# Optimization experiments

Hardware: AMD Instinct MI355X
Metric: run time of the kernel (lower is better)

Reference implementation:

```python
import jax, jax.numpy as jnp
import numpy as np

BATCH, H, W = 1024, 32, 32
NUM_PIXELS = H * W                 # 1024
NUM_WIRES = 11                     # ceil(log2(1024)) + 1
NUM_LAYERS = 8

_CNOT = jnp.array([[1, 0, 0, 0],
                   [0, 1, 0, 0],
                   [0, 0, 0, 1],
                   [0, 0, 1, 0]], dtype=jnp.complex64)


def setup_inputs() -> dict:
    key = jax.random.key(0)
    k1, k2, k3 = jax.random.split(key, 3)
    image = jax.random.uniform(k1, (BATCH, 1, H, W), dtype=jnp.float32)
    label = jax.random.normal(k2, (BATCH,), dtype=jnp.float32)
    weights = jax.random.normal(k3, (NUM_LAYERS, NUM_WIRES, 3), dtype=jnp.float32) * 0.4
    return {"image": image, "label": label, "weights": weights}


def _apply_1q(state, U, w):
    # state: (B,) + (2,)*n ; U: (2,2) shared or (B,2,2) per-batch
    st = jnp.moveaxis(state, w + 1, -1)
    if U.ndim == 3:
        out = jnp.einsum('bij,b...j->b...i', U, st)
    else:
        out = jnp.einsum('ij,...j->...i', U, st)
    return jnp.moveaxis(out, -1, w + 1)


def _apply_cnot(state, c, t):
    last = state.ndim - 1
    st = jnp.moveaxis(state, (c + 1, t + 1), (last - 1, last))
    sh = st.shape
    st = st.reshape(sh[:-2] + (4,)) @ _CNOT.T
    st = st.reshape(sh)
    return jnp.moveaxis(st, (last - 1, last), (c + 1, t + 1))


def _rot(phi, theta, omega):
    # PennyLane Rot = RZ(omega) RY(theta) RZ(phi)
    c = jnp.cos(theta / 2).astype(jnp.complex64)
    s = jnp.sin(theta / 2).astype(jnp.complex64)
    ep = jnp.exp(-0.5j * (phi + omega))
    em = jnp.exp(0.5j * (phi - omega))
    return jnp.array([[ep * c, -em * s],
                      [jnp.conj(em) * s, jnp.conj(ep) * c]])


def _circuit(image, label, weights):
    B = image.shape[0]
    x = image.reshape(B, NUM_PIXELS)
    # AmplitudeEmbedding(normalize=True) on wires 0..NUM_WIRES-2; ancilla wire in |0>
    psi = x / jnp.linalg.norm(x, axis=1, keepdims=True)
    state = jnp.zeros((B, 2 ** NUM_WIRES), jnp.complex64)
    state = state.at[:, ::2].set(psi.astype(jnp.complex64))  # ancilla = least-significant wire
    state = state.reshape((B,) + (2,) * NUM_WIRES)

    # RX(label) on the last wire (per-batch angle)
    c = jnp.cos(label / 2).astype(jnp.complex64)
    s = (-1j * jnp.sin(label / 2)).astype(jnp.complex64)
    rx = jnp.stack([jnp.stack([c, s], -1), jnp.stack([s, c], -1)], -2)  # (B,2,2)
    state = _apply_1q(state, rx, NUM_WIRES - 1)

    # weights remapped as in the module
    wr = jnp.pi * jnp.tanh(weights)

    # StronglyEntanglingLayers: per layer, Rot on every wire then ring of CNOTs with range r
    for l in range(NUM_LAYERS):
        for q in range(NUM_WIRES):
            state = _apply_1q(state, _rot(wr[l, q, 0], wr[l, q, 1], wr[l, q, 2]), q)
        r = (l % (NUM_WIRES - 1)) + 1
        for q in range(NUM_WIRES):
            state = _apply_cnot(state, q, (q + r) % NUM_WIRES)

    probs = jnp.abs(state.reshape(B, -1)) ** 2          # (B, 2048)
    probs = probs[:, ::2]                               # ancilla == 0 outcomes, (B, 1024)
    out = probs * NUM_PIXELS                            # decode: undo 1/num_pixels scale
    return out.reshape(B, 1, H, W)


def reference(image, label, weights):
    return _circuit(image, label, weights)
```

## Files before the change

kernel.cpp:

```cpp
#include <hip/hip_runtime.h>
#include <math.h>

#define NW 11
#define NL 8
#define NPIX 1024
#define TPB 256

typedef float f2 __attribute__((ext_vector_type(2)));
typedef float f4 __attribute__((ext_vector_type(4)));

struct PermTab { int fe[NL][8]; int d[NL][8]; };

__host__ __device__ inline int fmap_h(int m, int r) {
    for (int q = 0; q < NW; ++q) {
        int pc = 10 - q;
        int qq = q + r; if (qq >= NW) qq -= NW;
        int pt = 10 - qq;
        m ^= ((m >> pc) & 1) << pt;
    }
    return m;
}

__host__ __device__ constexpr int SW(int e) {
    return e ^ (((e >> 3) & 7) << 1) ^ (((e >> 6) & 1) << 3);
}

template<int B>
__device__ __forceinline__ void gate8(f2 (&v)[8], const f2* __restrict__ g) {
    f2 c0 = g[0], c1 = g[1], c2 = g[2], c3 = g[3];
    f2 c4 = g[4], c5 = g[5], c6 = g[6], c7 = g[7];
    #pragma unroll
    for (int s = 0; s < 8; ++s) {
        if (s & B) continue;
        f2 v0 = v[s], v1 = v[s | B];
        f2 w0 = v0.yx, w1 = v1.yx;
        f2 o0 = __builtin_elementwise_fma(c3, w1,
                 __builtin_elementwise_fma(c2, v1,
                  __builtin_elementwise_fma(c1, w0, c0 * v0)));
        f2 o1 = __builtin_elementwise_fma(c7, w1,
                 __builtin_elementwise_fma(c6, v1,
                  __builtin_elementwise_fma(c5, w0, c4 * v0)));
        v[s] = o0; v[s | B] = o1;
    }
}

__global__ void gates_kernel(const float* __restrict__ weights, f2* __restrict__ gw) {
    int t = threadIdx.x;
    if (t < NL * NW) {
        const float* w = weights + t * 3;
        const float PI = 3.14159265358979323846f;
        float phi   = PI * tanhf(w[0]);
        float theta = PI * tanhf(w[1]);
        float omega = PI * tanhf(w[2]);
        float ct = cosf(0.5f * theta), st = sinf(0.5f * theta);
        float a  = 0.5f * (phi + omega), bb = 0.5f * (phi - omega);
        float ca = cosf(a), sa = sinf(a), cb = cosf(bb), sb = sinf(bb);
        float u00r =  ca * ct, u00i = -sa * ct;
        float u01r = -cb * st, u01i = -sb * st;
        float u10r =  cb * st, u10i = -sb * st;
        float u11r =  ca * ct, u11i =  sa * ct;
        f2* g = gw + t * 8;
        g[0] = (f2){u00r, u00r}; g[1] = (f2){-u00i, u00i};
        g[2] = (f2){u01r, u01r}; g[3] = (f2){-u01i, u01i};
        g[4] = (f2){u10r, u10r}; g[5] = (f2){-u10i, u10i};
        g[6] = (f2){u11r, u11r}; g[7] = (f2){-u11i, u11i};
    }
}

__global__ __launch_bounds__(TPB) void pqc_kernel(
    const float* __restrict__ image, const float* __restrict__ label,
    const f2* __restrict__ gw, float* __restrict__ out, PermTab pt)
{
    __shared__ __align__(16) f2 sS[2048];
    __shared__ float sRed[4];

    const int b = blockIdx.x, t = threadIdx.x;

    const f4 x = ((const f4*)(image + (size_t)b * NPIX))[t];
    float ss = x.x * x.x + x.y * x.y + x.z * x.z + x.w * x.w;
    #pragma unroll
    for (int off = 32; off >= 1; off >>= 1) ss += __shfl_down(ss, off);
    if ((t & 63) == 0) sRed[t >> 6] = ss;
    __syncthreads();
    const float inv = 1.0f / sqrtf(sRed[0] + sRed[1] + sRed[2] + sRed[3]);

    const float lab = label[b];
    const float cl = cosf(0.5f * lab), sl = sinf(0.5f * lab);

    f2 v[8];
    {
        float ps[4] = {x.x, x.y, x.z, x.w};
        #pragma unroll
        for (int m = 0; m < 4; ++m) {
            float p = ps[m] * inv;
            v[2 * m]     = (f2){cl * p, 0.f};
            v[2 * m + 1] = (f2){0.f, -sl * p};
        }
    }

    const int swb0 = SW(t << 3);
    const int swb1 = SW((t & 7) | ((t >> 3) << 6));
    const int swb2 = SW((t & 63) | ((t >> 6) << 9));
    const int swb3 = SW(t << 1);

    for (int l = 0; l < NL; ++l) {
        const f2* G = gw + (size_t)l * NW * 8;

        if (l) {
            #pragma unroll
            for (int k = 0; k < 4; ++k) {
                f4 w = *(const f4*)&sS[swb0 ^ SW(2 * k)];
                v[2 * k] = w.xy; v[2 * k + 1] = w.zw;
            }
        }
        gate8<1>(v, G + 10 * 8);
        gate8<2>(v, G +  9 * 8);
        gate8<4>(v, G +  8 * 8);
        #pragma unroll
        for (int k = 0; k < 4; ++k) {
            f4 w; w.xy = v[2 * k]; w.zw = v[2 * k + 1];
            *(f4*)&sS[swb0 ^ SW(2 * k)] = w;
        }
        __syncthreads();

        {
            #pragma unroll
            for (int s = 0; s < 8; ++s) v[s] = sS[swb1 ^ SW(s << 3)];
            gate8<1>(v, G + 7 * 8);
            gate8<2>(v, G + 6 * 8);
            gate8<4>(v, G + 5 * 8);
            #pragma unroll
            for (int s = 0; s < 8; ++s) sS[swb1 ^ SW(s << 3)] = v[s];
        }
        __syncthreads();

        {
            #pragma unroll
            for (int s = 0; s < 8; ++s) v[s] = sS[swb2 ^ SW(s << 6)];
            gate8<1>(v, G + 4 * 8);
            gate8<2>(v, G + 3 * 8);
            gate8<4>(v, G + 2 * 8);
            #pragma unroll
            for (int s = 0; s < 8; ++s) sS[swb2 ^ SW(s << 6)] = v[s];
        }
        __syncthreads();

        {
            #pragma unroll
            for (int k = 0; k < 4; ++k) {
                f4 w = *(const f4*)&sS[swb3 ^ ((k & 1) << 9) ^ ((k >> 1) << 10)];
                v[2 * k] = w.xy; v[2 * k + 1] = w.zw;
            }
            gate8<2>(v, G + 1 * 8);
            gate8<4>(v, G + 0 * 8);
            int msw = 0;
            #pragma unroll
            for (int k2 = 0; k2 < 8; ++k2)
                msw ^= ((t >> k2) & 1) ? pt.fe[l][k2] : 0;
            #pragma unroll
            for (int s = 0; s < 8; ++s) sS[msw ^ pt.d[l][s]] = v[s];
        }
        __syncthreads();
    }

    {
        f4 o;
        #pragma unroll
        for (int k = 0; k < 4; ++k) {
            f2 a = sS[swb0 ^ SW(2 * k)];
            ((float*)&o)[k] = (a.x * a.x + a.y * a.y) * (float)NPIX;
        }
        ((f4*)(out + (size_t)b * NPIX))[t] = o;
    }
}

extern "C" void kernel_launch(void* const* d_in, const int* in_sizes, int n_in,
                              void* d_out, int out_size, void* d_ws, size_t ws_size,
                              hipStream_t stream) {
    const float* image   = (const float*)d_in[0];
    const float* label   = (const float*)d_in[1];
    const float* weights = (const float*)d_in[2];
    float* out = (float*)d_out;
    f2* gw = (f2*)d_ws;

    PermTab pt;
    for (int l = 0; l < NL; ++l) {
        int r = l + 1;
        for (int k = 0; k < 8; ++k)
            pt.fe[l][k] = SW(fmap_h(1 << (k + 1), r));
        for (int s = 0; s < 8; ++s) {
            int m = 0;
            if (s & 1) m ^= fmap_h(1,       r);
            if (s & 2) m ^= fmap_h(1 << 9,  r);
            if (s & 4) m ^= fmap_h(1 << 10, r);
            pt.d[l][s] = SW(m);
        }
    }

    int batch = in_sizes[1];
    gates_kernel<<<1, 128, 0, stream>>>(weights, gw);
    pqc_kernel<<<batch, TPB, 0, stream>>>(image, label, gw, out, pt);
}
```

Measured before the change: 45.06 us.

## Make early layer phases wave-local and double-buffer state to cut block barriers

Rearranges which amplitudes each thread owns so that the first three gate phases of a layer only exchange data within a 64-lane wavefront. This lets those phases use s_waitcnt plus a sched_barrier instead of __syncthreads. Shared state is double-buffered so the permuted CNOT write-back targets the other buffer, which removes one more barrier. Each layer drops from four block barriers to two, at the cost of twice the LDS per block and new swizzle patterns that may cause bank conflicts. Correctness relies on the wave-locality of the index mappings and on wave-synchronous execution.

```diff
diff --git a/kernel.cpp b/kernel.cpp
--- a/kernel.cpp
+++ b/kernel.cpp
@@ -22,7 +22,7 @@
 }
 
 __host__ __device__ constexpr int SW(int e) {
-    return e ^ (((e >> 3) & 7) << 1) ^ (((e >> 6) & 1) << 3);
+    return e ^ (((e >> 6) & 7) << 1);
 }
 
 template<int B>
@@ -71,7 +71,7 @@
     const float* __restrict__ image, const float* __restrict__ label,
     const f2* __restrict__ gw, float* __restrict__ out, PermTab pt)
 {
-    __shared__ __align__(16) f2 sS[2048];
+    __shared__ __align__(16) f2 sS[2 * 2048];
     __shared__ float sRed[4];
 
     const int b = blockIdx.x, t = threadIdx.x;
@@ -98,77 +98,79 @@
         }
     }
 
-    const int swb0 = SW(t << 3);
-    const int swb1 = SW((t & 7) | ((t >> 3) << 6));
-    const int swb2 = SW((t & 63) | ((t >> 6) << 9));
-    const int swb3 = SW(t << 1);
-
+    const int swbA = (((t >> 6) << 9) | ((t & 63) << 3)) ^ (((t >> 3) & 7) << 1);
+    const int swbB = ((t & 7) | (((t >> 3) & 7) << 6) | ((t >> 6) << 9))
+                   ^ (((t >> 3) & 7) << 1);
+    const int swbC = (t & 63) | ((t >> 6) << 9);
+    const int swbD = (t << 1) ^ (((t >> 5) & 7) << 1);
+
+    int offS = 0;
     for (int l = 0; l < NL; ++l) {
         const f2* G = gw + (size_t)l * NW * 8;
+        const int offT = offS ^ 2048;
+        const int bA = offS ^ swbA, bB = offS ^ swbB;
+        const int bC = offS ^ swbC, bD = offS ^ swbD;
 
         if (l) {
             #pragma unroll
-            for (int k = 0; k < 4; ++k) {
-                f4 w = *(const f4*)&sS[swb0 ^ SW(2 * k)];
-                v[2 * k] = w.xy; v[2 * k + 1] = w.zw;
+            for (int j = 0; j < 4; ++j) {
+                f4 w = *(const f4*)&sS[bA ^ (2 * j)];
+                v[2 * j] = w.xy; v[2 * j + 1] = w.zw;
             }
         }
         gate8<1>(v, G + 10 * 8);
         gate8<2>(v, G +  9 * 8);
         gate8<4>(v, G +  8 * 8);
         #pragma unroll
-        for (int k = 0; k < 4; ++k) {
-            f4 w; w.xy = v[2 * k]; w.zw = v[2 * k + 1];
-            *(f4*)&sS[swb0 ^ SW(2 * k)] = w;
-        }
+        for (int j = 0; j < 4; ++j) {
+            f4 w; w.xy = v[2 * j]; w.zw = v[2 * j + 1];
+            *(f4*)&sS[bA ^ (2 * j)] = w;
+        }
+        asm volatile("s_waitcnt lgkmcnt(0)" ::: "memory");
+        __builtin_amdgcn_sched_barrier(0);
+
+        #pragma unroll
+        for (int s = 0; s < 8; ++s) v[s] = sS[bB ^ (s << 3)];
+        gate8<1>(v, G + 7 * 8);
+        gate8<2>(v, G + 6 * 8);
+        gate8<4>(v, G + 5 * 8);
+        #pragma unroll
+        for (int s = 0; s < 8; ++s) sS[bB ^ (s << 3)] = v[s];
+        asm volatile("s_waitcnt lgkmcnt(0)" ::: "memory");
+        __builtin_amdgcn_sched_barrier(0);
+
+        #pragma unroll
+        for (int s = 0; s < 8; ++s) v[s] = sS[bC ^ (s << 6) ^ (s << 1)];
+        gate8<1>(v, G + 4 * 8);
+        gate8<2>(v, G + 3 * 8);
+        gate8<4>(v, G + 2 * 8);
+        #pragma unroll
+        for (int s = 0; s < 8; ++s) sS[bC ^ (s << 6) ^ (s << 1)] = v[s];
         __syncthreads();
 
-        {
-            #pragma unroll
-            for (int s = 0; s < 8; ++s) v[s] = sS[swb1 ^ SW(s << 3)];
-            gate8<1>(v, G + 7 * 8);
-            gate8<2>(v, G + 6 * 8);
-            gate8<4>(v, G + 5 * 8);
-            #pragma unroll
-            for (int s = 0; s < 8; ++s) sS[swb1 ^ SW(s << 3)] = v[s];
-        }
+        #pragma unroll
+        for (int j = 0; j < 4; ++j) {
+            f4 w = *(const f4*)&sS[bD ^ ((j & 1) << 9) ^ ((j >> 1) << 10)];
+            v[2 * j] = w.xy; v[2 * j + 1] = w.zw;
+        }
+        gate8<2>(v, G + 1 * 8);
+        gate8<4>(v, G + 0 * 8);
+        int msw = offT;
+        #pragma unroll
+        for (int k2 = 0; k2 < 8; ++k2)
+            msw ^= ((t >> k2) & 1) ? pt.fe[l][k2] : 0;
+        #pragma unroll
+        for (int s = 0; s < 8; ++s) sS[msw ^ pt.d[l][s]] = v[s];
         __syncthreads();
-
-        {
-            #pragma unroll
-            for (int s = 0; s < 8; ++s) v[s] = sS[swb2 ^ SW(s << 6)];
-            gate8<1>(v, G + 4 * 8);
-            gate8<2>(v, G + 3 * 8);
-            gate8<4>(v, G + 2 * 8);
-            #pragma unroll
-            for (int s = 0; s < 8; ++s) sS[swb2 ^ SW(s << 6)] = v[s];
-        }
-        __syncthreads();
-
-        {
-            #pragma unroll
-            for (int k = 0; k < 4; ++k) {
-                f4 w = *(const f4*)&sS[swb3 ^ ((k & 1) << 9) ^ ((k >> 1) << 10)];
-                v[2 * k] = w.xy; v[2 * k + 1] = w.zw;
-            }
-            gate8<2>(v, G + 1 * 8);
-            gate8<4>(v, G + 0 * 8);
-            int msw = 0;
-            #pragma unroll
-            for (int k2 = 0; k2 < 8; ++k2)
-                msw ^= ((t >> k2) & 1) ? pt.fe[l][k2] : 0;
-            #pragma unroll
-            for (int s = 0; s < 8; ++s) sS[msw ^ pt.d[l][s]] = v[s];
-        }
-        __syncthreads();
+        offS = offT;
     }
 
     {
         f4 o;
         #pragma unroll
-        for (int k = 0; k < 4; ++k) {
-            f2 a = sS[swb0 ^ SW(2 * k)];
-            ((float*)&o)[k] = (a.x * a.x + a.y * a.y) * (float)NPIX;
+        for (int j = 0; j < 4; ++j) {
+            f4 w = *(const f4*)&sS[(offS ^ swbA) ^ (2 * j)];
+            ((float*)&o)[j] = (w.x * w.x + w.y * w.y) * (float)NPIX;
         }
         ((f4*)(out + (size_t)b * NPIX))[t] = o;
     }
```

After: 56.05 us. 1.24x slower.

## Apply mid-wire gates via DPP and permlane swaps to cut LDS round trips

Applied to the files above, without the earlier changes.

Each wave now applies single-qubit gates to wires held across lanes directly in registers, using DPP cross-lane fetches and v_permlane16/32_swap exchanges. This replaces two of the four shared-memory transpose stages and their barriers per layer. Two LDS buffers are used, so each layer needs only two barriers, and the swizzle pattern is redefined to match. The cost is more ALU work per gate (every lane computes a full 2x2 product with a fetched partner value), plus reliance on MI355-specific permlane-swap instructions.

```diff
diff --git a/kernel.cpp b/kernel.cpp
--- a/kernel.cpp
+++ b/kernel.cpp
@@ -11,7 +11,7 @@
 
 struct PermTab { int fe[NL][8]; int d[NL][8]; };
 
-__host__ __device__ inline int fmap_h(int m, int r) {
+static inline int fmap_h(int m, int r) {
     for (int q = 0; q < NW; ++q) {
         int pc = 10 - q;
         int qq = q + r; if (qq >= NW) qq -= NW;
@@ -22,25 +22,73 @@
 }
 
 __host__ __device__ constexpr int SW(int e) {
-    return e ^ (((e >> 3) & 7) << 1) ^ (((e >> 6) & 1) << 3);
-}
-
-template<int B>
-__device__ __forceinline__ void gate8(f2 (&v)[8], const f2* __restrict__ g) {
-    f2 c0 = g[0], c1 = g[1], c2 = g[2], c3 = g[3];
-    f2 c4 = g[4], c5 = g[5], c6 = g[6], c7 = g[7];
+    return e ^ (((e >> 4) & 7) << 1);
+}
+
+#define FMA2 __builtin_elementwise_fma
+
+template<int CTRL>
+__device__ __forceinline__ float dpp_f(float x) {
+    int xi = __float_as_int(x);
+    int r  = __builtin_amdgcn_update_dpp(xi, xi, CTRL, 0xF, 0xF, false);
+    return __int_as_float(r);
+}
+template<int CTRL>
+__device__ __forceinline__ f2 dpp2(f2 v) {
+    return (f2){dpp_f<CTRL>(v.x), dpp_f<CTRL>(v.y)};
+}
+
+template<int MODE>
+__device__ __forceinline__ f2 bfetch(f2 v, int L) {
+    if constexpr (MODE == 0) return dpp2<0x128>(v);
+    else if constexpr (MODE == 1) {
+        f2 fwd = dpp2<0x104>(v);
+        f2 bwd = dpp2<0x114>(v);
+        return (L & 4) ? bwd : fwd;
+    }
+    else if constexpr (MODE == 2) return dpp2<0x4E>(v);
+    else return dpp2<0xB1>(v);
+}
+
+__device__ __forceinline__ void swap32(f2& a, f2& b) {
+    float ax = a.x, ay = a.y, bx = b.x, by = b.y;
+    asm volatile("v_permlane32_swap_b32 %0, %1" : "+v"(ax), "+v"(bx));
+    asm volatile("v_permlane32_swap_b32 %0, %1" : "+v"(ay), "+v"(by));
+    a = (f2){ax, ay}; b = (f2){bx, by};
+}
+__device__ __forceinline__ void swap16(f2& a, f2& b) {
+    float ax = a.x, ay = a.y, bx = b.x, by = b.y;
+    asm volatile("v_permlane16_swap_b32 %0, %1" : "+v"(ax), "+v"(bx));
+    asm volatile("v_permlane16_swap_b32 %0, %1" : "+v"(ay), "+v"(by));
+    a = (f2){ax, ay}; b = (f2){bx, by};
+}
+
+template<int M>
+__device__ __forceinline__ void gateR8(f2 (&X)[8], const f2* __restrict__ g) {
+    const f2 c0 = g[0], c1 = g[1], c2 = g[2], c3 = g[3];
+    const f2 c4 = g[4], c5 = g[5], c6 = g[6], c7 = g[7];
     #pragma unroll
     for (int s = 0; s < 8; ++s) {
-        if (s & B) continue;
-        f2 v0 = v[s], v1 = v[s | B];
-        f2 w0 = v0.yx, w1 = v1.yx;
-        f2 o0 = __builtin_elementwise_fma(c3, w1,
-                 __builtin_elementwise_fma(c2, v1,
-                  __builtin_elementwise_fma(c1, w0, c0 * v0)));
-        f2 o1 = __builtin_elementwise_fma(c7, w1,
-                 __builtin_elementwise_fma(c6, v1,
-                  __builtin_elementwise_fma(c5, w0, c4 * v0)));
-        v[s] = o0; v[s | B] = o1;
+        if (s & M) continue;
+        const int s1 = s | M;
+        f2 v0 = X[s], v1 = X[s1];
+        f2 v0y = v0.yx, v1y = v1.yx;
+        X[s]  = FMA2(c3, v1y, FMA2(c2, v1, FMA2(c1, v0y, c0 * v0)));
+        X[s1] = FMA2(c7, v1y, FMA2(c6, v1, FMA2(c5, v0y, c4 * v0)));
+    }
+}
+
+template<int LBIT, int MODE>
+__device__ __forceinline__ void gateL8(f2 (&X)[8], const f2* __restrict__ g, int L) {
+    const bool sb = (L >> LBIT) & 1;
+    const f2 a0 = sb ? g[6] : g[0], a1 = sb ? g[7] : g[1];
+    const f2 b0 = sb ? g[4] : g[2], b1 = sb ? g[5] : g[3];
+    #pragma unroll
+    for (int s = 0; s < 8; ++s) {
+        f2 v = X[s];
+        f2 p = bfetch<MODE>(v, L);
+        f2 vy = v.yx, py = p.yx;
+        X[s] = FMA2(b1, py, FMA2(b0, p, FMA2(a1, vy, a0 * v)));
     }
 }
 
@@ -71,10 +119,12 @@
     const float* __restrict__ image, const float* __restrict__ label,
     const f2* __restrict__ gw, float* __restrict__ out, PermTab pt)
 {
-    __shared__ __align__(16) f2 sS[2048];
+    __shared__ __align__(16) f2 sA[2048];
+    __shared__ __align__(16) f2 sB[2048];
     __shared__ float sRed[4];
 
     const int b = blockIdx.x, t = threadIdx.x;
+    const int L = t & 63, w = t >> 6;
 
     const f4 x = ((const f4*)(image + (size_t)b * NPIX))[t];
     float ss = x.x * x.x + x.y * x.y + x.z * x.z + x.w * x.w;
@@ -87,88 +137,83 @@
     const float lab = label[b];
     const float cl = cosf(0.5f * lab), sl = sinf(0.5f * lab);
 
-    f2 v[8];
+    f2 X[8];
     {
         float ps[4] = {x.x, x.y, x.z, x.w};
         #pragma unroll
         for (int m = 0; m < 4; ++m) {
             float p = ps[m] * inv;
-            v[2 * m]     = (f2){cl * p, 0.f};
-            v[2 * m + 1] = (f2){0.f, -sl * p};
-        }
-    }
-
-    const int swb0 = SW(t << 3);
-    const int swb1 = SW((t & 7) | ((t >> 3) << 6));
-    const int swb2 = SW((t & 63) | ((t >> 6) << 9));
-    const int swb3 = SW(t << 1);
+            X[2 * m]     = (f2){cl * p, 0.f};
+            X[2 * m + 1] = (f2){0.f, -sl * p};
+        }
+    }
+
+    const int e0b  = (L << 3) | (w << 9);
+    const int swb0 = e0b ^ (((e0b >> 4) & 7) << 1);
+    const int eb = ((L & 1) << 3) | (((L >> 1) & 1) << 4) | (((L >> 2) & 1) << 5)
+                 | (((L >> 3) & 1) << 6) | (((L >> 4) & 1) << 2)
+                 | (((L >> 5) & 1) << 1) | (w << 9);
+    const int swb1 = eb ^ (((eb >> 4) & 7) << 1);
+    const int bD   = t << 1;
+    const int swbD = bD ^ (((bD >> 4) & 7) << 1);
 
     for (int l = 0; l < NL; ++l) {
         const f2* G = gw + (size_t)l * NW * 8;
 
         if (l) {
             #pragma unroll
-            for (int k = 0; k < 4; ++k) {
-                f4 w = *(const f4*)&sS[swb0 ^ SW(2 * k)];
-                v[2 * k] = w.xy; v[2 * k + 1] = w.zw;
+            for (int jh = 0; jh < 4; ++jh) {
+                f4 wv = *(const f4*)&sB[swb0 ^ (jh << 1)];
+                X[2 * jh] = wv.xy; X[2 * jh + 1] = wv.zw;
             }
         }
-        gate8<1>(v, G + 10 * 8);
-        gate8<2>(v, G +  9 * 8);
-        gate8<4>(v, G +  8 * 8);
+
+        gateR8<1>(X, G + 10 * 8);
+        gateR8<2>(X, G +  9 * 8);
+        gateR8<4>(X, G +  8 * 8);
+        gateL8<0, 3>(X, G + 7 * 8, L);
+        gateL8<1, 2>(X, G + 6 * 8, L);
+        gateL8<2, 1>(X, G + 5 * 8, L);
+        gateL8<3, 0>(X, G + 4 * 8, L);
+        swap16(X[0], X[4]); swap16(X[1], X[5]);
+        swap16(X[2], X[6]); swap16(X[3], X[7]);
+        gateR8<4>(X, G + 3 * 8);
+        swap32(X[0], X[2]); swap32(X[1], X[3]);
+        swap32(X[4], X[6]); swap32(X[5], X[7]);
+        gateR8<2>(X, G + 2 * 8);
+
+        #pragma unroll
+        for (int jh = 0; jh < 4; ++jh) {
+            f4 wv; wv.xy = X[2 * jh]; wv.zw = X[2 * jh + 1];
+            *(f4*)&sA[swb1 ^ ((jh & 1) << 8) ^ ((jh >> 1) << 7)] = wv;
+        }
+        __syncthreads();
+
+        f2 Y[8];
         #pragma unroll
         for (int k = 0; k < 4; ++k) {
-            f4 w; w.xy = v[2 * k]; w.zw = v[2 * k + 1];
-            *(f4*)&sS[swb0 ^ SW(2 * k)] = w;
-        }
+            f4 wv = *(const f4*)&sA[swbD ^ ((k & 1) << 9) ^ ((k >> 1) << 10)];
+            Y[2 * k] = wv.xy; Y[2 * k + 1] = wv.zw;
+        }
+        gateR8<2>(Y, G + 1 * 8);
+        gateR8<4>(Y, G + 0 * 8);
+        int msw = 0;
+        #pragma unroll
+        for (int k2 = 0; k2 < 8; ++k2)
+            msw ^= ((t >> k2) & 1) ? pt.fe[l][k2] : 0;
+        #pragma unroll
+        for (int s = 0; s < 8; ++s) sB[msw ^ pt.d[l][s]] = Y[s];
         __syncthreads();
-
-        {
-            #pragma unroll
-            for (int s = 0; s < 8; ++s) v[s] = sS[swb1 ^ SW(s << 3)];
-            gate8<1>(v, G + 7 * 8);
-            gate8<2>(v, G + 6 * 8);
-            gate8<4>(v, G + 5 * 8);
-            #pragma unroll
-            for (int s = 0; s < 8; ++s) sS[swb1 ^ SW(s << 3)] = v[s];
-        }
-        __syncthreads();
-
-        {
-            #pragma unroll
-            for (int s = 0; s < 8; ++s) v[s] = sS[swb2 ^ SW(s << 6)];
-            gate8<1>(v, G + 4 * 8);
-            gate8<2>(v, G + 3 * 8);
-            gate8<4>(v, G + 2 * 8);
-            #pragma unroll
-            for (int s = 0; s < 8; ++s) sS[swb2 ^ SW(s << 6)] = v[s];
-        }
-        __syncthreads();
-
-        {
-            #pragma unroll
-            for (int k = 0; k < 4; ++k) {
-                f4 w = *(const f4*)&sS[swb3 ^ ((k & 1) << 9) ^ ((k >> 1) << 10)];
-                v[2 * k] = w.xy; v[2 * k + 1] = w.zw;
-            }
-            gate8<2>(v, G + 1 * 8);
-            gate8<4>(v, G + 0 * 8);
-            int msw = 0;
-            #pragma unroll
-            for (int k2 = 0; k2 < 8; ++k2)
-                msw ^= ((t >> k2) & 1) ? pt.fe[l][k2] : 0;
-            #pragma unroll
-            for (int s = 0; s < 8; ++s) sS[msw ^ pt.d[l][s]] = v[s];
-        }
-        __syncthreads();
     }
 
     {
+        const int eo  = t << 3;
+        const int swO = eo ^ (((eo >> 4) & 7) << 1);
         f4 o;
         #pragma unroll
-        for (int k = 0; k < 4; ++k) {
-            f2 a = sS[swb0 ^ SW(2 * k)];
-            ((float*)&o)[k] = (a.x * a.x + a.y * a.y) * (float)NPIX;
+        for (int m = 0; m < 4; ++m) {
+            f4 wv = *(const f4*)&sB[swO ^ (m << 1)];
+            ((float*)&o)[m] = (wv.x * wv.x + wv.y * wv.y) * (float)NPIX;
         }
         ((f4*)(out + (size_t)b * NPIX))[t] = o;
     }
```

Result: slower. 53.05 us (+17.7%).
